# Kernel optimization log

Measured on AMD Instinct MI355X. Metric: run time of the kernel, lower is better.

The kernel has to match this reference:

```python
import jax, jax.numpy as jnp
import numpy as np

N, K, H, W = 2048, 8, 128, 128
G = 50              # glimpse size (50x50 from tem_rnn input 50*50)
ENC = 100           # glimpse encoder output (relation_rnn input arithmetic)
HID = 256
D_REL = ENC + (3 + 50) * 2 + HID          # 462
D_TEM = G * G + (3 + 50) * 2 + HID        # 2862


def _lin(k, out_d, in_d, scale=0.02):
    k1, k2 = jax.random.split(k)
    return (jax.random.normal(k1, (out_d, in_d), jnp.float32) * scale,
            jax.random.normal(k2, (out_d,), jnp.float32) * scale)


def _lstm_params(k, in_d, hid):
    k1, k2, k3, k4 = jax.random.split(k, 4)
    s = 0.02
    return (jax.random.normal(k1, (4 * hid, in_d), jnp.float32) * s,
            jax.random.normal(k2, (4 * hid, hid), jnp.float32) * s,
            jax.random.normal(k3, (4 * hid,), jnp.float32) * s,
            jax.random.normal(k4, (4 * hid,), jnp.float32) * s)


def lstm_cell(x, h, c, Wih, Whh, bih, bhh):
    g = x @ Wih.T + h @ Whh.T + (bih + bhh)
    i, f, gg, o = jnp.split(g, 4, axis=-1)
    i, f, o = jax.nn.sigmoid(i), jax.nn.sigmoid(f), jax.nn.sigmoid(o)
    c2 = f * c + i * jnp.tanh(gg)
    return o * jnp.tanh(c2), c2


def _bilinear_one(im, py, px):
    # im [H,W]; py,px [G,G] pixel coords; zeros padding like torch grid_sample
    x0 = jnp.floor(px); y0 = jnp.floor(py)
    wx1 = px - x0; wy1 = py - y0
    x0i = x0.astype(jnp.int32); y0i = y0.astype(jnp.int32)

    def gather(yi, xi):
        valid = (yi >= 0) & (yi < H) & (xi >= 0) & (xi < W)
        v = im[jnp.clip(yi, 0, H - 1), jnp.clip(xi, 0, W - 1)]
        return jnp.where(valid, v, 0.0)

    return ((1 - wy1) * (1 - wx1) * gather(y0i, x0i)
            + (1 - wy1) * wx1 * gather(y0i, x0i + 1)
            + wy1 * (1 - wx1) * gather(y0i + 1, x0i)
            + wy1 * wx1 * gather(y0i + 1, x0i + 1))


def stn_glimpse(z_where, img):
    # z_where [n,3] = (scale, tx, ty); theta = [[s,0,tx],[0,s,ty]] (attentive_stn_encode)
    s, tx, ty = z_where[:, 0], z_where[:, 1], z_where[:, 2]
    lin = jnp.linspace(-1.0, 1.0, G)
    gy, gx = jnp.meshgrid(lin, lin, indexing='ij')           # [G,G]
    px = (s[:, None, None] * gx + tx[:, None, None] + 1.0) * 0.5 * (W - 1)
    py = (s[:, None, None] * gy + ty[:, None, None] + 1.0) * 0.5 * (H - 1)
    out = jax.vmap(_bilinear_one)(img, py, px)               # [n,G,G]
    return out.reshape(out.shape[0], G * G)


def setup_inputs() -> dict:
    key = jax.random.key(0)
    ks = jax.random.split(key, 16)
    inp = {
        'img': jax.random.uniform(ks[0], (N, H, W), jnp.float32),
        'z_what_last': jax.random.normal(ks[1], (N, K, 50), jnp.float32),
        'z_where_last': jax.random.normal(ks[2], (N, K, 3), jnp.float32) * 0.3,
        'z_pres_last': jnp.ones((N, K, 1), jnp.float32),
        'hidden_last': jax.random.normal(ks[3], (N, K, HID), jnp.float32),
    }
    inp['W_loca'], inp['b_loca'] = _lin(ks[4], 3, HID)
    inp['Wg'], inp['bg'] = _lin(ks[5], ENC, G * G)
    (inp['Wih_rel'], inp['Whh_rel'], inp['bih_rel'], inp['bhh_rel']) = _lstm_params(ks[6], D_REL, HID)
    (inp['Wih_tem'], inp['Whh_tem'], inp['bih_tem'], inp['bhh_tem']) = _lstm_params(ks[7], D_TEM, HID)
    inp['Wm_wh'], inp['bm_wh'] = _lin(ks[8], 3, HID + 3)
    inp['Ws_wh'], inp['bs_wh'] = _lin(ks[9], 3, HID + 3)
    inp['Wm_wt'], inp['bm_wt'] = _lin(ks[10], 50, 50 + HID + HID)
    inp['Ws_wt'], inp['bs_wt'] = _lin(ks[11], 50, 50 + HID + HID)
    inp['Wm_pr'], inp['bm_pr'] = _lin(ks[12], 1, 50 + 3 + HID + HID)
    inp['Ws_pr'], inp['bs_pr'] = _lin(ks[13], 1, 50 + 3 + HID + HID)
    return inp


def reference(img, z_what_last, z_where_last, z_pres_last, hidden_last,
              W_loca, b_loca, Wg, bg,
              Wih_rel, Whh_rel, bih_rel, bhh_rel,
              Wih_tem, Whh_tem, bih_tem, bhh_tem,
              Wm_wh, bm_wh, Ws_wh, bs_wh,
              Wm_wt, bm_wt, Ws_wt, bs_wt,
              Wm_pr, bm_pr, Ws_pr, bs_pr):
    n = img.shape[0]

    def step(carry, xs):
        h_r, c_r, pzw, pzwhat = carry
        zwl, zwhatl, zpl, hl = xs   # [n,3],[n,50],[n,1],[n,256]
        # prop_loca: relu(linear(hidden)) + z_where_last
        zwb = jax.nn.relu(hl @ W_loca.T + b_loca) + zwl
        # STN glimpse + encode (bias pass)
        enc = jax.nn.relu(stn_glimpse(zwb, img) @ Wg.T + bg)        # [n,100]
        rin = jnp.concatenate([enc, zwl, pzw, zwhatl, pzwhat, hl], -1)  # [n,462]
        h_r2, c_r2 = lstm_cell(rin, h_r, c_r, Wih_rel, Whh_rel, bih_rel, bhh_rel)
        # z_where: latent predictor mean (eval mode)
        zw = jnp.concatenate([zwl, h_r2], -1) @ Wm_wh.T + bm_wh      # [n,3]
        # second STN glimpse with sampled where
        g2 = stn_glimpse(zw, img)                                    # [n,2500]
        tin = jnp.concatenate([g2, zw, pzw, zwhatl, pzwhat, hl], -1) # [n,2862]
        h_t, c_t = lstm_cell(tin, h_r2, c_r2, Wih_tem, Whh_tem, bih_tem, bhh_tem)
        # z_what mean
        zwhat = jnp.concatenate([zwhatl, h_r2, h_t], -1) @ Wm_wt.T + bm_wt  # [n,50]
        # z_pres: deterministic expectation of Bernoulli(mean*std) * previous pres
        zp_cal = jnp.concatenate([zwhat, zw, h_r2, h_t], -1)
        p = jax.nn.sigmoid(zp_cal @ Wm_pr.T + bm_pr) * jax.nn.sigmoid(zp_cal @ Ws_pr.T + bs_pr)
        zp = p * zpl                                                 # [n,1]
        return (h_r2, c_r2, zw, zwhat), (zwhat, zw, zp, h_t)

    carry0 = (jnp.zeros((n, HID), img.dtype), jnp.zeros((n, HID), img.dtype),
              jnp.zeros((n, 3), img.dtype), jnp.zeros((n, 50), img.dtype))
    xs = (jnp.swapaxes(z_where_last, 0, 1), jnp.swapaxes(z_what_last, 0, 1),
          jnp.swapaxes(z_pres_last, 0, 1), jnp.swapaxes(hidden_last, 0, 1))
    _, (zwhat_s, zw_s, zp_s, ht_s) = jax.lax.scan(step, carry0, xs)
    z_what = jnp.swapaxes(zwhat_s, 0, 1)   # [n,K,50]
    z_where = jnp.swapaxes(zw_s, 0, 1)     # [n,K,3]
    z_pres = jnp.swapaxes(zp_s, 0, 1)      # [n,K,1]
    h_temp = jnp.swapaxes(ht_s, 0, 1)      # [n,K,256]
    return z_what, z_where, z_pres, h_temp
```

## Files before the change

kernel.cpp:

```cpp
#include <hip/hip_runtime.h>
#include <hip/hip_bf16.h>
#include <math.h>

typedef __attribute__((ext_vector_type(8))) short bf16x8;
typedef __attribute__((ext_vector_type(4))) float f32x4;
using bf16 = __hip_bfloat16;

constexpr int NN   = 2048;
constexpr int KO   = 8;
constexpr int IH   = 128, IW = 128;
constexpr int GS   = 50;
constexpr int GG2  = GS*GS;
constexpr int HIDD = 256;
constexpr int RIN_LD = 768;
constexpr int TIN_LD = 3136;
constexpr int G1_LD  = 2560;

__device__ __forceinline__ float sigm(float x) { return 1.f/(1.f+expf(-x)); }

template<int OUT_BF16, int RELU>
__global__ __launch_bounds__(256, 2) void mfma_gemm(
    const bf16* __restrict__ A, int lda, int Kd,
    const bf16* __restrict__ Wt, int ldw, int M,
    const float* __restrict__ b1, const float* __restrict__ b2,
    void* __restrict__ Cout, int ldc)
{
    __shared__ bf16x8 As16[512];
    __shared__ bf16x8 Bs16[512];
    const int tid  = threadIdx.x;
    const int n0   = blockIdx.y*64;
    const int m0   = blockIdx.x*64;
    const int wave = tid>>6, lane = tid&63;
    const int wy   = wave>>1, wx = wave&1;

    const int row = tid>>2, part = tid&3;
    const bf16* Ap = A + (size_t)(n0+row)*lda + part*8;
    const int   wm = m0 + row;
    const bool  wok = wm < M;
    const bf16* Wp = Wt + (size_t)(wok ? wm : 0)*ldw + part*8;
    const int dst0 = ((row>>4)*2+0)*64 + part*16 + (row&15);
    const int dst1 = dst0 + 64;

    f32x4 acc[2][2] = {};
    const bf16x8 z8 = {};
    bf16x8 pa0 = *(const bf16x8*)Ap;
    bf16x8 pa1 = *(const bf16x8*)(Ap + 32);
    bf16x8 pw0 = *(const bf16x8*)Wp;
    bf16x8 pw1 = *(const bf16x8*)(Wp + 32);

    for (int k0 = 0; k0 < Kd; k0 += 64) {
        __syncthreads();
        As16[dst0] = pa0;
        As16[dst1] = pa1;
        Bs16[dst0] = wok ? pw0 : z8;
        Bs16[dst1] = wok ? pw1 : z8;
        __syncthreads();
        if (k0 + 64 < Kd) {
            pa0 = *(const bf16x8*)(Ap + k0 + 64);
            pa1 = *(const bf16x8*)(Ap + k0 + 96);
            pw0 = *(const bf16x8*)(Wp + k0 + 64);
            pw1 = *(const bf16x8*)(Wp + k0 + 96);
        }
        bf16x8 av[2][2], bv[2][2];
        #pragma unroll
        for (int i=0;i<2;i++)
            #pragma unroll
            for (int h=0;h<2;h++) av[i][h] = As16[((wy*2+i)*2+h)*64 + lane];
        #pragma unroll
        for (int j=0;j<2;j++)
            #pragma unroll
            for (int h=0;h<2;h++) bv[j][h] = Bs16[((wx*2+j)*2+h)*64 + lane];
        #pragma unroll
        for (int h=0;h<2;h++)
            #pragma unroll
            for (int i=0;i<2;i++)
                #pragma unroll
                for (int j=0;j<2;j++)
                    acc[i][j] = __builtin_amdgcn_mfma_f32_16x16x32_bf16(av[i][h], bv[j][h], acc[i][j], 0, 0, 0);
    }

    const int q = lane>>4, r = lane&15;
    #pragma unroll
    for (int j=0;j<2;j++) {
        int col = m0 + wx*32 + j*16 + r;
        if (col < M) {
            float bias = 0.f;
            if (b1) bias += b1[col];
            if (b2) bias += b2[col];
            #pragma unroll
            for (int i=0;i<2;i++) {
                #pragma unroll
                for (int reg=0;reg<4;reg++) {
                    float v = acc[i][j][reg] + bias;
                    if (RELU) v = fmaxf(v, 0.f);
                    size_t idx = (size_t)(n0 + wy*32 + i*16 + q*4 + reg)*ldc + col;
                    if (OUT_BF16) ((bf16*)Cout)[idx] = __float2bfloat16(v);
                    else          ((float*)Cout)[idx] = v;
                }
            }
        }
    }
}

__device__ __forceinline__ void glimpse_points(const float* __restrict__ im,
                                               float s, float tx, float ty,
                                               bf16* __restrict__ drow) {
    const float GXS = 2.0f/49.0f;
    const float txp = tx + 1.0f, typ = ty + 1.0f;
    for (int p2 = threadIdx.x; p2 < 1250; p2 += 256) {
        int i = p2 / 25;
        int j = (p2 - i*25) * 2;
        float gy  = fmaf((float)i, GXS, -1.0f);
        float py  = fmaf(s, gy, typ) * 63.5f;
        float y0f = floorf(py); float fy = py - y0f; int y0 = (int)y0f;
        float wy0 = ((unsigned)y0     < 128u) ? (1.f - fy) : 0.f;
        float wy1 = ((unsigned)(y0+1) < 128u) ? fy         : 0.f;
        const float* r0 = im + min(max(y0,  0),127)*IW;
        const float* r1 = im + min(max(y0+1,0),127)*IW;
        float gxa = fmaf((float)j, GXS, -1.0f);
        float pxa = fmaf(s, gxa, txp) * 63.5f;
        float xa0f = floorf(pxa); float fa = pxa - xa0f; int xa0 = (int)xa0f;
        float wa0 = ((unsigned)xa0     < 128u) ? (1.f - fa) : 0.f;
        float wa1 = ((unsigned)(xa0+1) < 128u) ? fa         : 0.f;
        int xa0c = min(max(xa0,  0),127), xa1c = min(max(xa0+1,0),127);
        float gxb = fmaf((float)(j+1), GXS, -1.0f);
        float pxb = fmaf(s, gxb, txp) * 63.5f;
        float xb0f = floorf(pxb); float fb = pxb - xb0f; int xb0 = (int)xb0f;
        float wb0 = ((unsigned)xb0     < 128u) ? (1.f - fb) : 0.f;
        float wb1 = ((unsigned)(xb0+1) < 128u) ? fb         : 0.f;
        int xb0c = min(max(xb0,  0),127), xb1c = min(max(xb0+1,0),127);

        float va = fmaf(wy1, fmaf(wa0, r1[xa0c], wa1*r1[xa1c]),
                   wy0 *     fmaf(wa0, r0[xa0c], wa1*r0[xa1c]));
        float vb = fmaf(wy1, fmaf(wb0, r1[xb0c], wb1*r1[xb1c]),
                   wy0 *     fmaf(wb0, r0[xb0c], wb1*r0[xb1c]));

        bf16 b0 = __float2bfloat16(va), b1 = __float2bfloat16(vb);
        unsigned short u0, u1;
        __builtin_memcpy(&u0, &b0, 2); __builtin_memcpy(&u1, &b1, 2);
        *(unsigned int*)(drow + i*GS + j) = (unsigned)u0 | ((unsigned)u1 << 16);
    }
}

__global__ __launch_bounds__(256) void glimpse_batch(const float* __restrict__ img,
                                                     const float* __restrict__ z,
                                                     bf16* __restrict__ dst, int ldd) {
    int b = blockIdx.x;
    const float* im = img + (size_t)(b & (NN-1))*IH*IW;
    glimpse_points(im, z[b*3+0], z[b*3+1], z[b*3+2], dst + (size_t)b*ldd);
}

__global__ __launch_bounds__(256) void glimpse2_fused(const float* __restrict__ img,
                                                      const float* __restrict__ zw_cur,
                                                      const float* __restrict__ zw_prev,
                                                      const float* __restrict__ zwhat_prev,
                                                      const float* __restrict__ z_what_last,
                                                      const float* __restrict__ hidden_last,
                                                      bf16* __restrict__ tin, int k) {
    int n = blockIdx.x;
    const float* im = img + (size_t)n*IH*IW;
    float s  = zw_cur[n*3+0];
    float tx = zw_cur[n*3+1];
    float ty = zw_cur[n*3+2];
    bf16* trow = tin + (size_t)n*TIN_LD;
    glimpse_points(im, s, tx, ty, trow);
    for (int c = threadIdx.x; c < 362; c += 256) {
        float v;
        if      (c <   3) v = (c==0) ? s : ((c==1) ? tx : ty);
        else if (c <   6) v = zw_prev[n*3 + c-3];
        else if (c <  56) v = z_what_last[((size_t)n*KO + k)*50 + c-6];
        else if (c < 106) v = zwhat_prev[n*50 + c-56];
        else              v = hidden_last[((size_t)n*KO + k)*HIDD + c-106];
        trow[2500 + c] = __float2bfloat16(v);
    }
}

__global__ void zero_f32(float* __restrict__ p, int n) {
    int i = blockIdx.x*blockDim.x + threadIdx.x;
    if (i < n) p[i] = 0.f;
}

__global__ void repack_w(const float* __restrict__ s1, int K1,
                         const float* __restrict__ s2, int K2,
                         bf16* __restrict__ dst, int ldd, int M) {
    int gid = blockIdx.x*blockDim.x + threadIdx.x;
    if (gid >= M*ldd) return;
    int m = gid / ldd, c = gid - m*ldd;
    float v = 0.f;
    if (c < K1)           v = s1[(size_t)m*K1 + c];
    else if (c < K1+K2)   v = s2[(size_t)m*K2 + (c-K1)];
    dst[gid] = __float2bfloat16(v);
}

__global__ void zwb_all_kernel(const float* __restrict__ hidden_last,
                               const float* __restrict__ z_where_last,
                               const float* __restrict__ Wl, const float* __restrict__ bl,
                               float* __restrict__ zwb_all) {
    int gid = blockIdx.x*blockDim.x + threadIdx.x;
    if (gid >= KO*NN*3) return;
    int j = gid % 3; int rn = gid/3; int n = rn & (NN-1); int s = rn >> 11;
    const float* hl = hidden_last + ((size_t)n*KO + s)*HIDD;
    const float* w  = Wl + j*HIDD;
    float acc = bl[j];
    for (int i=0;i<HIDD;i++) acc = fmaf(hl[i], w[i], acc);
    zwb_all[gid] = fmaxf(acc, 0.f) + z_where_last[((size_t)n*KO + s)*3 + j];
}

__global__ void fill_rin_static(bf16* __restrict__ rin,
                                const float* __restrict__ z_where_last,
                                const float* __restrict__ z_what_last,
                                const float* __restrict__ hidden_last,
                                int base, int CH) {
    int gid = blockIdx.x*blockDim.x + threadIdx.x;
    if (gid >= CH*NN*309) return;
    int c = gid % 309; int rn = gid/309; int n = rn & (NN-1); int sl = rn >> 11;
    int k = base + sl;
    float v; int col;
    if (c < 3)       { col = 100 + c;      v = z_where_last[((size_t)n*KO + k)*3 + c]; }
    else if (c < 53) { col = 106 + (c-3);  v = z_what_last[((size_t)n*KO + k)*50 + (c-3)]; }
    else             { col = 206 + (c-53); v = hidden_last[((size_t)n*KO + k)*HIDD + (c-53)]; }
    rin[(size_t)rn*RIN_LD + col] = __float2bfloat16(v);
}

__global__ void zero_rin_carry(bf16* __restrict__ rin0) {
    int gid = blockIdx.x*blockDim.x + threadIdx.x;
    if (gid >= NN*309) return;
    int c = gid % 309, n = gid/309;
    int col = (c < 3) ? 103+c : ((c < 53) ? 156+(c-3) : 462+(c-53));
    rin0[(size_t)n*RIN_LD + col] = __float2bfloat16(0.f);
}

__global__ __launch_bounds__(256) void rel_fused(
    const float* __restrict__ gates, float* __restrict__ h_r, float* __restrict__ c_r,
    const float* __restrict__ z_where_last,
    const float* __restrict__ Wm_wh, const float* __restrict__ bm_wh,
    float* __restrict__ zw_cur, float* __restrict__ out_zwhere,
    bf16* __restrict__ rin_next, bf16* __restrict__ tin, int k)
{
    __shared__ float hs[256];
    int n = blockIdx.x, j = threadIdx.x;
    const float* g = gates + (size_t)n*1024;
    float ig = sigm(g[j]);
    float fg = sigm(g[256+j]);
    float gg = tanhf(g[512+j]);
    float og = sigm(g[768+j]);
    int cidx = n*256 + j;
    float c2 = fg*c_r[cidx] + ig*gg;
    float hv = og*tanhf(c2);
    c_r[cidx] = c2;
    h_r[cidx] = hv;
    hs[j] = hv;
    bf16 hb = __float2bfloat16(hv);
    rin_next[(size_t)n*RIN_LD + 462 + j] = hb;
    tin[(size_t)n*TIN_LD + 2862 + j]     = hb;
    __syncthreads();
    int w = j >> 6, lane = j & 63;
    if (w < 3) {
        const float* wt = Wm_wh + w*259;
        float s = 0.f;
        for (int i = lane; i < 256; i += 64) s = fmaf(hs[i], wt[3+i], s);
        #pragma unroll
        for (int off = 32; off; off >>= 1) s += __shfl_down(s, off);
        if (lane == 0) {
            const float* zwl = z_where_last + ((size_t)n*KO + k)*3;
            float acc = bm_wh[w] + s;
            for (int i = 0; i < 3; i++) acc = fmaf(zwl[i], wt[i], acc);
            zw_cur[n*3+w] = acc;
            out_zwhere[((size_t)n*KO + k)*3 + w] = acc;
            rin_next[(size_t)n*RIN_LD + 103 + w] = __float2bfloat16(acc);
        }
    }
}

__global__ __launch_bounds__(256) void tem_fused(
    const float* __restrict__ gates, const float* __restrict__ c_r, const float* __restrict__ h_r,
    const float* __restrict__ z_what_last,
    const float* __restrict__ Wm_wt, const float* __restrict__ bm_wt,
    const float* __restrict__ Wm_pr, const float* __restrict__ bm_pr,
    const float* __restrict__ Ws_pr, const float* __restrict__ bs_pr,
    const float* __restrict__ zw_cur, const float* __restrict__ z_pres_last,
    float* __restrict__ zwhat_cur, float* __restrict__ out_zwhat,
    float* __restrict__ out_htemp, float* __restrict__ out_zpres,
    bf16* __restrict__ rin_next, int k)
{
    __shared__ float L[615];
    int n = blockIdx.x, j = threadIdx.x;
    const float* g = gates + (size_t)n*1024;
    float ig = sigm(g[j]);
    float fg = sigm(g[256+j]);
    float gg = tanhf(g[512+j]);
    float og = sigm(g[768+j]);
    float c2 = fg*c_r[n*256+j] + ig*gg;
    float hv = og*tanhf(c2);
    out_htemp[((size_t)n*KO + k)*HIDD + j] = hv;
    L[309+j] = hv;
    L[53+j]  = h_r[n*256+j];
    if (j < 50)      L[j]  = z_what_last[((size_t)n*KO + k)*50 + j];
    else if (j < 53) L[j]  = zw_cur[n*3 + (j-50)];
    __syncthreads();
    if (j < 200) {
        int m = j >> 2, part = j & 3;
        const float* wt = Wm_wt + m*562;
        float s = 0.f;
        for (int i = part; i < 562; i += 4) {
            float v = (i < 50) ? L[i] : L[i+3];
            s = fmaf(v, wt[i], s);
        }
        s += __shfl_down(s, 2);
        s += __shfl_down(s, 1);
        if (part == 0) {
            float acc = s + bm_wt[m];
            zwhat_cur[n*50+m] = acc;
            out_zwhat[((size_t)n*KO + k)*50 + m] = acc;
            rin_next[(size_t)n*RIN_LD + 156 + m] = __float2bfloat16(acc);
            L[565+m] = acc;
        }
    }
    __syncthreads();
    if (j < 64) {
        float s1 = 0.f, s2 = 0.f;
        for (int i = j; i < 565; i += 64) {
            float v = (i < 50) ? L[565+i] : L[i];
            s1 = fmaf(v, Wm_pr[i], s1);
            s2 = fmaf(v, Ws_pr[i], s2);
        }
        #pragma unroll
        for (int off = 32; off; off >>= 1) { s1 += __shfl_down(s1,off); s2 += __shfl_down(s2,off); }
        if (j == 0) {
            float p = sigm(s1 + bm_pr[0]) * sigm(s2 + bs_pr[0]);
            out_zpres[(size_t)n*KO + k] = p * z_pres_last[(size_t)n*KO + k];
        }
    }
}

extern "C" void kernel_launch(void* const* d_in, const int* in_sizes, int n_in,
                              void* d_out, int out_size, void* d_ws, size_t ws_size,
                              hipStream_t stream) {
    (void)in_sizes; (void)n_in; (void)out_size;
    const float* img          = (const float*)d_in[0];
    const float* z_what_last  = (const float*)d_in[1];
    const float* z_where_last = (const float*)d_in[2];
    const float* z_pres_last  = (const float*)d_in[3];
    const float* hidden_last  = (const float*)d_in[4];
    const float* W_loca = (const float*)d_in[5];
    const float* b_loca = (const float*)d_in[6];
    const float* Wg     = (const float*)d_in[7];
    const float* bg     = (const float*)d_in[8];
    const float* Wih_rel = (const float*)d_in[9];
    const float* Whh_rel = (const float*)d_in[10];
    const float* bih_rel = (const float*)d_in[11];
    const float* bhh_rel = (const float*)d_in[12];
    const float* Wih_tem = (const float*)d_in[13];
    const float* Whh_tem = (const float*)d_in[14];
    const float* bih_tem = (const float*)d_in[15];
    const float* bhh_tem = (const float*)d_in[16];
    const float* Wm_wh = (const float*)d_in[17];
    const float* bm_wh = (const float*)d_in[18];
    const float* Wm_wt = (const float*)d_in[21];
    const float* bm_wt = (const float*)d_in[22];
    const float* Wm_pr = (const float*)d_in[25];
    const float* bm_pr = (const float*)d_in[26];
    const float* Ws_pr = (const float*)d_in[27];
    const float* bs_pr = (const float*)d_in[28];

    char* base_p = (char*)d_ws;
    size_t off = 0;
    auto carve = [&](size_t bytes) -> char* {
        char* r = base_p + off;
        off += (bytes + 255) & ~(size_t)255;
        return r;
    };
    bf16*  tin      = (bf16*) carve((size_t)NN*TIN_LD*2);
    float* gates    = (float*)carve((size_t)NN*1024*4);
    bf16*  W_tem    = (bf16*) carve((size_t)1024*TIN_LD*2);
    bf16*  W_rel    = (bf16*) carve((size_t)1024*RIN_LD*2);
    bf16*  Wg_bf    = (bf16*) carve((size_t)100*G1_LD*2);
    float* zwb_all  = (float*)carve((size_t)KO*NN*3*4);
    float* h_r      = (float*)carve((size_t)NN*HIDD*4);
    float* c_r      = (float*)carve((size_t)NN*HIDD*4);
    float* zw1      = (float*)carve((size_t)NN*3*4);
    float* zwhat1   = (float*)carve((size_t)NN*50*4);
    float* zw0      = (float*)carve((size_t)NN*3*4);
    float* zwhat0   = (float*)carve((size_t)NN*50*4);
    size_t fixed_bytes = off;

    int CH = 1;
    for (int cand : {8, 4, 2}) {
        size_t need = fixed_bytes
                    + (((size_t)cand*NN*G1_LD*2 + 255) & ~(size_t)255)
                    + (((size_t)cand*NN*RIN_LD*2 + 255) & ~(size_t)255);
        if (need <= ws_size) { CH = cand; break; }
    }
    bf16* g1 = nullptr; int g1ld;
    bf16* rin;
    if (CH > 1) {
        g1   = (bf16*)carve((size_t)CH*NN*G1_LD*2);
        rin  = (bf16*)carve((size_t)CH*NN*RIN_LD*2);
        g1ld = G1_LD;
    } else {
        rin  = (bf16*)carve((size_t)NN*RIN_LD*2);
        g1   = tin;
        g1ld = TIN_LD;
    }

    float* out        = (float*)d_out;
    float* out_zwhat  = out;
    float* out_zwhere = out + (size_t)NN*KO*50;
    float* out_zpres  = out_zwhere + (size_t)NN*KO*3;
    float* out_htemp  = out_zpres + (size_t)NN*KO;

    {
        int nz = NN*(HIDD + 3 + 50);
        zero_f32<<<(nz+255)/256, 256, 0, stream>>>(c_r, nz);
    }
    zero_rin_carry<<<(NN*309+255)/256, 256, 0, stream>>>(rin);
    repack_w<<<((1024*RIN_LD)+255)/256, 256, 0, stream>>>(Wih_rel, 462, Whh_rel, 256, W_rel, RIN_LD, 1024);
    repack_w<<<((1024*TIN_LD)+255)/256, 256, 0, stream>>>(Wih_tem, 2862, Whh_tem, 256, W_tem, TIN_LD, 1024);
    repack_w<<<((100*G1_LD)+255)/256, 256, 0, stream>>>(Wg, 2500, nullptr, 0, Wg_bf, G1_LD, 100);
    zwb_all_kernel<<<(KO*NN*3+255)/256, 256, 0, stream>>>(hidden_last, z_where_last, W_loca, b_loca, zwb_all);

    for (int cbase = 0; cbase < KO; cbase += CH) {
        fill_rin_static<<<(CH*NN*309+255)/256, 256, 0, stream>>>(rin, z_where_last, z_what_last, hidden_last, cbase, CH);
        glimpse_batch<<<CH*NN, 256, 0, stream>>>(img, zwb_all + (size_t)cbase*NN*3, g1, g1ld);
        mfma_gemm<1,1><<<dim3(2, CH*32), 256, 0, stream>>>(g1, g1ld, G1_LD, Wg_bf, G1_LD, 100, bg, nullptr, rin, RIN_LD);

        for (int s = 0; s < CH; ++s) {
            int k = cbase + s;
            bf16* rin_k  = rin + (size_t)s*NN*RIN_LD;
            bf16* rin_nx = rin + (size_t)((s+1)%CH)*NN*RIN_LD;
            float* zw_cur     = (k & 1) ? zw1 : zw0;
            float* zw_prev    = (k & 1) ? zw0 : zw1;
            float* zwhat_cur  = (k & 1) ? zwhat1 : zwhat0;
            float* zwhat_prev = (k & 1) ? zwhat0 : zwhat1;

            mfma_gemm<0,0><<<dim3(16, 32), 256, 0, stream>>>(rin_k, RIN_LD, RIN_LD, W_rel, RIN_LD, 1024, bih_rel, bhh_rel, gates, 1024);
            rel_fused<<<NN, 256, 0, stream>>>(gates, h_r, c_r, z_where_last, Wm_wh, bm_wh, zw_cur, out_zwhere, rin_nx, tin, k);
            glimpse2_fused<<<NN, 256, 0, stream>>>(img, zw_cur, zw_prev, zwhat_prev, z_what_last, hidden_last, tin, k);
            mfma_gemm<0,0><<<dim3(16, 32), 256, 0, stream>>>(tin, TIN_LD, TIN_LD, W_tem, TIN_LD, 1024, bih_tem, bhh_tem, gates, 1024);
            tem_fused<<<NN, 256, 0, stream>>>(gates, c_r, h_r, z_what_last, Wm_wt, bm_wt, Wm_pr, bm_pr, Ws_pr, bs_pr,
                                              zw_cur, z_pres_last, zwhat_cur, out_zwhat, out_htemp, out_zpres, rin_nx, k);
        }
    }
}
```

Measured before the change: 1.348 ms.

## Fuse LSTM gate epilogue into GEMM and stage glimpse rows in LDS

The LSTM weight rows are reordered so each 64-column GEMM tile holds all four gates for 16 hidden units. The gate nonlinearities and cell update then run in the GEMM epilogue, which removes the fp32 gates buffer round trip and the separate rel/tem elementwise kernels. The z_where projection moves into the glimpse kernel. Glimpse sampling first copies the needed image rows into shared memory, and zwb_all is rewritten as a wave reduction. The cost is more shared memory per block, which may lower occupancy, and an extra epilogue sync in the GEMM.

```diff
diff --git a/kernel.cpp b/kernel.cpp
--- a/kernel.cpp
+++ b/kernel.cpp
@@ -10,23 +10,30 @@
 constexpr int KO   = 8;
 constexpr int IH   = 128, IW = 128;
 constexpr int GS   = 50;
-constexpr int GG2  = GS*GS;
 constexpr int HIDD = 256;
 constexpr int RIN_LD = 768;
 constexpr int TIN_LD = 3136;
 constexpr int G1_LD  = 2560;
+constexpr int GROWS  = 80;
 
 __device__ __forceinline__ float sigm(float x) { return 1.f/(1.f+expf(-x)); }
 
-template<int OUT_BF16, int RELU>
+template<int MODE>
 __global__ __launch_bounds__(256, 2) void mfma_gemm(
     const bf16* __restrict__ A, int lda, int Kd,
     const bf16* __restrict__ Wt, int ldw, int M,
     const float* __restrict__ b1, const float* __restrict__ b2,
-    void* __restrict__ Cout, int ldc)
+    const float* __restrict__ bint,
+    void* __restrict__ Cout, int ldc,
+    float* __restrict__ c_r, float* __restrict__ h_out,
+    bf16* __restrict__ rin_next, bf16* __restrict__ tin_,
+    float* __restrict__ out_htemp, int kstep)
 {
-    __shared__ bf16x8 As16[512];
-    __shared__ bf16x8 Bs16[512];
+    __shared__ __align__(16) char shraw[68*64*4];
+    bf16x8* As16 = (bf16x8*)shraw;
+    bf16x8* Bs16 = As16 + 512;
+    float*  Gt   = (float*)shraw;
+
     const int tid  = threadIdx.x;
     const int n0   = blockIdx.y*64;
     const int m0   = blockIdx.x*64;
@@ -80,94 +87,197 @@
     }
 
     const int q = lane>>4, r = lane&15;
-    #pragma unroll
-    for (int j=0;j<2;j++) {
-        int col = m0 + wx*32 + j*16 + r;
-        if (col < M) {
-            float bias = 0.f;
-            if (b1) bias += b1[col];
-            if (b2) bias += b2[col];
+    if (MODE == 1) {
+        #pragma unroll
+        for (int j=0;j<2;j++) {
+            int col = m0 + wx*32 + j*16 + r;
+            if (col < M) {
+                float bias = 0.f;
+                if (b1) bias += b1[col];
+                if (b2) bias += b2[col];
+                #pragma unroll
+                for (int i=0;i<2;i++)
+                    #pragma unroll
+                    for (int reg=0;reg<4;reg++) {
+                        float v = fmaxf(acc[i][j][reg] + bias, 0.f);
+                        ((bf16*)Cout)[(size_t)(n0 + wy*32 + i*16 + q*4 + reg)*ldc + col] = __float2bfloat16(v);
+                    }
+            }
+        }
+    } else {
+        __syncthreads();
+        #pragma unroll
+        for (int j=0;j<2;j++) {
+            int colL = wx*32 + j*16 + r;
+            float bias = bint[m0 + colL];
             #pragma unroll
-            for (int i=0;i<2;i++) {
+            for (int i=0;i<2;i++)
                 #pragma unroll
-                for (int reg=0;reg<4;reg++) {
-                    float v = acc[i][j][reg] + bias;
-                    if (RELU) v = fmaxf(v, 0.f);
-                    size_t idx = (size_t)(n0 + wy*32 + i*16 + q*4 + reg)*ldc + col;
-                    if (OUT_BF16) ((bf16*)Cout)[idx] = __float2bfloat16(v);
-                    else          ((float*)Cout)[idx] = v;
-                }
+                for (int reg=0;reg<4;reg++)
+                    Gt[(wy*32 + i*16 + q*4 + reg)*68 + colL] = acc[i][j][reg] + bias;
+        }
+        __syncthreads();
+        #pragma unroll
+        for (int it=0; it<4; ++it) {
+            int item = tid + it*256;
+            int rowL = item >> 4, u16 = item & 15;
+            f32x4 gv = *(const f32x4*)&Gt[rowL*68 + u16*4];
+            float ig = sigm(gv[0]);
+            float fg = sigm(gv[1]);
+            float gg = tanhf(gv[2]);
+            float og = sigm(gv[3]);
+            int n = n0 + rowL, u = (m0>>2) + u16;
+            size_t cidx = (size_t)n*HIDD + u;
+            float c2 = fg*c_r[cidx] + ig*gg;
+            float hv = og*tanhf(c2);
+            if (MODE == 2) {
+                c_r[cidx] = c2;
+                h_out[cidx] = hv;
+                bf16 hb = __float2bfloat16(hv);
+                rin_next[(size_t)n*RIN_LD + 462 + u] = hb;
+                tin_[(size_t)n*TIN_LD + 2862 + u]    = hb;
+            } else {
+                h_out[cidx] = hv;
+                out_htemp[((size_t)n*KO + kstep)*HIDD + u] = hv;
             }
         }
     }
 }
 
-__device__ __forceinline__ void glimpse_points(const float* __restrict__ im,
-                                               float s, float tx, float ty,
-                                               bf16* __restrict__ drow) {
+__device__ __forceinline__ void glimpse_core(const float* __restrict__ im,
+                                             float s, float tx, float ty,
+                                             bf16* __restrict__ drow,
+                                             float* __restrict__ rows) {
     const float GXS = 2.0f/49.0f;
     const float txp = tx + 1.0f, typ = ty + 1.0f;
-    for (int p2 = threadIdx.x; p2 < 1250; p2 += 256) {
-        int i = p2 / 25;
-        int j = (p2 - i*25) * 2;
-        float gy  = fmaf((float)i, GXS, -1.0f);
-        float py  = fmaf(s, gy, typ) * 63.5f;
-        float y0f = floorf(py); float fy = py - y0f; int y0 = (int)y0f;
-        float wy0 = ((unsigned)y0     < 128u) ? (1.f - fy) : 0.f;
-        float wy1 = ((unsigned)(y0+1) < 128u) ? fy         : 0.f;
-        const float* r0 = im + min(max(y0,  0),127)*IW;
-        const float* r1 = im + min(max(y0+1,0),127)*IW;
-        float gxa = fmaf((float)j, GXS, -1.0f);
-        float pxa = fmaf(s, gxa, txp) * 63.5f;
-        float xa0f = floorf(pxa); float fa = pxa - xa0f; int xa0 = (int)xa0f;
-        float wa0 = ((unsigned)xa0     < 128u) ? (1.f - fa) : 0.f;
-        float wa1 = ((unsigned)(xa0+1) < 128u) ? fa         : 0.f;
-        int xa0c = min(max(xa0,  0),127), xa1c = min(max(xa0+1,0),127);
-        float gxb = fmaf((float)(j+1), GXS, -1.0f);
-        float pxb = fmaf(s, gxb, txp) * 63.5f;
-        float xb0f = floorf(pxb); float fb = pxb - xb0f; int xb0 = (int)xb0f;
-        float wb0 = ((unsigned)xb0     < 128u) ? (1.f - fb) : 0.f;
-        float wb1 = ((unsigned)(xb0+1) < 128u) ? fb         : 0.f;
-        int xb0c = min(max(xb0,  0),127), xb1c = min(max(xb0+1,0),127);
-
-        float va = fmaf(wy1, fmaf(wa0, r1[xa0c], wa1*r1[xa1c]),
-                   wy0 *     fmaf(wa0, r0[xa0c], wa1*r0[xa1c]));
-        float vb = fmaf(wy1, fmaf(wb0, r1[xb0c], wb1*r1[xb1c]),
-                   wy0 *     fmaf(wb0, r0[xb0c], wb1*r0[xb1c]));
-
-        bf16 b0 = __float2bfloat16(va), b1 = __float2bfloat16(vb);
-        unsigned short u0, u1;
-        __builtin_memcpy(&u0, &b0, 2); __builtin_memcpy(&u1, &b1, 2);
-        *(unsigned int*)(drow + i*GS + j) = (unsigned)u0 | ((unsigned)u1 << 16);
+    float pyA = fmaf(s, -1.f, typ)*63.5f;
+    float pyB = fmaf(s,  1.f, typ)*63.5f;
+    int ylo = (int)floorf(fminf(pyA, pyB));
+    int yhi = (int)floorf(fmaxf(pyA, pyB)) + 1;
+    ylo = min(max(ylo, 0), 127);
+    yhi = min(max(yhi, 0), 127);
+    int nrows = yhi - ylo + 1;
+
+    if (nrows <= GROWS) {
+        const float4* src = (const float4*)(im + ylo*IW);
+        float4* d4 = (float4*)rows;
+        int tot = nrows*(IW/4);
+        for (int t = threadIdx.x; t < tot; t += 256) d4[t] = src[t];
+        __syncthreads();
+        for (int p2 = threadIdx.x; p2 < 1250; p2 += 256) {
+            int i = p2 / 25, j = (p2 - i*25)*2;
+            float gy  = fmaf((float)i, GXS, -1.0f);
+            float py  = fmaf(s, gy, typ)*63.5f;
+            float y0f = floorf(py); float fy = py - y0f; int y0 = (int)y0f;
+            float wy0 = ((unsigned)y0     < 128u) ? (1.f - fy) : 0.f;
+            float wy1 = ((unsigned)(y0+1) < 128u) ? fy         : 0.f;
+            const float* r0 = rows + min(max(y0-ylo,   0), nrows-1)*IW;
+            const float* r1 = rows + min(max(y0+1-ylo, 0), nrows-1)*IW;
+            float gxa = fmaf((float)j, GXS, -1.0f);
+            float pxa = fmaf(s, gxa, txp)*63.5f;
+            float xa0f = floorf(pxa); float fa = pxa - xa0f; int xa0 = (int)xa0f;
+            float wa0 = ((unsigned)xa0     < 128u) ? (1.f - fa) : 0.f;
+            float wa1 = ((unsigned)(xa0+1) < 128u) ? fa         : 0.f;
+            int xa0c = min(max(xa0,  0),127), xa1c = min(max(xa0+1,0),127);
+            float gxb = fmaf((float)(j+1), GXS, -1.0f);
+            float pxb = fmaf(s, gxb, txp)*63.5f;
+            float xb0f = floorf(pxb); float fb = pxb - xb0f; int xb0 = (int)xb0f;
+            float wb0 = ((unsigned)xb0     < 128u) ? (1.f - fb) : 0.f;
+            float wb1 = ((unsigned)(xb0+1) < 128u) ? fb         : 0.f;
+            int xb0c = min(max(xb0,  0),127), xb1c = min(max(xb0+1,0),127);
+            float va = fmaf(wy1, fmaf(wa0, r1[xa0c], wa1*r1[xa1c]),
+                       wy0 *     fmaf(wa0, r0[xa0c], wa1*r0[xa1c]));
+            float vb = fmaf(wy1, fmaf(wb0, r1[xb0c], wb1*r1[xb1c]),
+                       wy0 *     fmaf(wb0, r0[xb0c], wb1*r0[xb1c]));
+            bf16 b0 = __float2bfloat16(va), b1 = __float2bfloat16(vb);
+            unsigned short u0, u1;
+            __builtin_memcpy(&u0, &b0, 2); __builtin_memcpy(&u1, &b1, 2);
+            *(unsigned int*)(drow + i*GS + j) = (unsigned)u0 | ((unsigned)u1 << 16);
+        }
+    } else {
+        for (int p2 = threadIdx.x; p2 < 1250; p2 += 256) {
+            int i = p2 / 25, j = (p2 - i*25)*2;
+            float gy  = fmaf((float)i, GXS, -1.0f);
+            float py  = fmaf(s, gy, typ)*63.5f;
+            float y0f = floorf(py); float fy = py - y0f; int y0 = (int)y0f;
+            float wy0 = ((unsigned)y0     < 128u) ? (1.f - fy) : 0.f;
+            float wy1 = ((unsigned)(y0+1) < 128u) ? fy         : 0.f;
+            const float* r0 = im + min(max(y0,  0),127)*IW;
+            const float* r1 = im + min(max(y0+1,0),127)*IW;
+            float gxa = fmaf((float)j, GXS, -1.0f);
+            float pxa = fmaf(s, gxa, txp)*63.5f;
+            float xa0f = floorf(pxa); float fa = pxa - xa0f; int xa0 = (int)xa0f;
+            float wa0 = ((unsigned)xa0     < 128u) ? (1.f - fa) : 0.f;
+            float wa1 = ((unsigned)(xa0+1) < 128u) ? fa         : 0.f;
+            int xa0c = min(max(xa0,  0),127), xa1c = min(max(xa0+1,0),127);
+            float gxb = fmaf((float)(j+1), GXS, -1.0f);
+            float pxb = fmaf(s, gxb, txp)*63.5f;
+            float xb0f = floorf(pxb); float fb = pxb - xb0f; int xb0 = (int)xb0f;
+            float wb0 = ((unsigned)xb0     < 128u) ? (1.f - fb) : 0.f;
+            float wb1 = ((unsigned)(xb0+1) < 128u) ? fb         : 0.f;
+            int xb0c = min(max(xb0,  0),127), xb1c = min(max(xb0+1,0),127);
+            float va = fmaf(wy1, fmaf(wa0, r1[xa0c], wa1*r1[xa1c]),
+                       wy0 *     fmaf(wa0, r0[xa0c], wa1*r0[xa1c]));
+            float vb = fmaf(wy1, fmaf(wb0, r1[xb0c], wb1*r1[xb1c]),
+                       wy0 *     fmaf(wb0, r0[xb0c], wb1*r0[xb1c]));
+            bf16 b0 = __float2bfloat16(va), b1 = __float2bfloat16(vb);
+            unsigned short u0, u1;
+            __builtin_memcpy(&u0, &b0, 2); __builtin_memcpy(&u1, &b1, 2);
+            *(unsigned int*)(drow + i*GS + j) = (unsigned)u0 | ((unsigned)u1 << 16);
+        }
     }
 }
 
 __global__ __launch_bounds__(256) void glimpse_batch(const float* __restrict__ img,
                                                      const float* __restrict__ z,
                                                      bf16* __restrict__ dst, int ldd) {
+    __shared__ float rows[GROWS*IW];
     int b = blockIdx.x;
     const float* im = img + (size_t)(b & (NN-1))*IH*IW;
-    glimpse_points(im, z[b*3+0], z[b*3+1], z[b*3+2], dst + (size_t)b*ldd);
-}
-
-__global__ __launch_bounds__(256) void glimpse2_fused(const float* __restrict__ img,
-                                                      const float* __restrict__ zw_cur,
-                                                      const float* __restrict__ zw_prev,
-                                                      const float* __restrict__ zwhat_prev,
-                                                      const float* __restrict__ z_what_last,
-                                                      const float* __restrict__ hidden_last,
-                                                      bf16* __restrict__ tin, int k) {
-    int n = blockIdx.x;
-    const float* im = img + (size_t)n*IH*IW;
-    float s  = zw_cur[n*3+0];
-    float tx = zw_cur[n*3+1];
-    float ty = zw_cur[n*3+2];
+    glimpse_core(im, z[b*3+0], z[b*3+1], z[b*3+2], dst + (size_t)b*ldd, rows);
+}
+
+__global__ __launch_bounds__(256) void glimpse2_zw(
+    const float* __restrict__ img, const float* __restrict__ h_r,
+    const float* __restrict__ z_where_last,
+    const float* __restrict__ Wm_wh, const float* __restrict__ bm_wh,
+    const float* __restrict__ zw_prev, const float* __restrict__ zwhat_prev,
+    const float* __restrict__ z_what_last, const float* __restrict__ hidden_last,
+    float* __restrict__ zw_cur, float* __restrict__ out_zwhere,
+    bf16* __restrict__ tin, bf16* __restrict__ rin_next, int k)
+{
+    __shared__ float rows[GROWS*IW];
+    __shared__ float hsv[HIDD];
+    __shared__ float zws[3];
+    int n = blockIdx.x, tid = threadIdx.x;
+    hsv[tid] = h_r[(size_t)n*HIDD + tid];
+    __syncthreads();
+    int wv = tid>>6, lane = tid&63;
+    if (wv < 3) {
+        const float* wt = Wm_wh + wv*259;
+        float sa = 0.f;
+        for (int i = lane; i < 256; i += 64) sa = fmaf(hsv[i], wt[3+i], sa);
+        #pragma unroll
+        for (int off=32; off; off>>=1) sa += __shfl_down(sa, off);
+        if (lane == 0) {
+            const float* zwl = z_where_last + ((size_t)n*KO + k)*3;
+            float acc = bm_wh[wv] + sa;
+            for (int i=0;i<3;i++) acc = fmaf(zwl[i], wt[i], acc);
+            zws[wv] = acc;
+            zw_cur[n*3+wv] = acc;
+            out_zwhere[((size_t)n*KO + k)*3 + wv] = acc;
+            bf16 ab = __float2bfloat16(acc);
+            rin_next[(size_t)n*RIN_LD + 103 + wv] = ab;
+            tin[(size_t)n*TIN_LD + 2500 + wv]     = ab;
+        }
+    }
+    __syncthreads();
+    float s = zws[0], tx = zws[1], ty = zws[2];
     bf16* trow = tin + (size_t)n*TIN_LD;
-    glimpse_points(im, s, tx, ty, trow);
-    for (int c = threadIdx.x; c < 362; c += 256) {
+    glimpse_core(img + (size_t)n*IH*IW, s, tx, ty, trow, rows);
+    for (int c = 3 + tid; c < 362; c += 256) {
         float v;
-        if      (c <   3) v = (c==0) ? s : ((c==1) ? tx : ty);
-        else if (c <   6) v = zw_prev[n*3 + c-3];
+        if      (c <   6) v = zw_prev[n*3 + c-3];
         else if (c <  56) v = z_what_last[((size_t)n*KO + k)*50 + c-6];
         else if (c < 106) v = zwhat_prev[n*50 + c-56];
         else              v = hidden_last[((size_t)n*KO + k)*HIDD + c-106];
@@ -192,18 +302,59 @@
     dst[gid] = __float2bfloat16(v);
 }
 
-__global__ void zwb_all_kernel(const float* __restrict__ hidden_last,
-                               const float* __restrict__ z_where_last,
-                               const float* __restrict__ Wl, const float* __restrict__ bl,
-                               float* __restrict__ zwb_all) {
+__global__ void repack_w_gates(const float* __restrict__ s1, int K1,
+                               const float* __restrict__ s2, int K2,
+                               bf16* __restrict__ dst, int ldd) {
     int gid = blockIdx.x*blockDim.x + threadIdx.x;
-    if (gid >= KO*NN*3) return;
-    int j = gid % 3; int rn = gid/3; int n = rn & (NN-1); int s = rn >> 11;
+    if (gid >= 1024*ldd) return;
+    int mp = gid / ldd, c = gid - mp*ldd;
+    int u = mp >> 2, g = mp & 3;
+    int m = g*256 + u;
+    float v = 0.f;
+    if (c < K1)           v = s1[(size_t)m*K1 + c];
+    else if (c < K1+K2)   v = s2[(size_t)m*K2 + (c-K1)];
+    dst[gid] = __float2bfloat16(v);
+}
+
+__global__ void repack_bias_gates(const float* __restrict__ b1, const float* __restrict__ b2,
+                                  float* __restrict__ dst) {
+    int mp = blockIdx.x*blockDim.x + threadIdx.x;
+    if (mp >= 1024) return;
+    int u = mp >> 2, g = mp & 3;
+    dst[mp] = b1[g*256+u] + b2[g*256+u];
+}
+
+__global__ __launch_bounds__(256) void zwb_all_v2(const float* __restrict__ hidden_last,
+                                                  const float* __restrict__ z_where_last,
+                                                  const float* __restrict__ Wl, const float* __restrict__ bl,
+                                                  float* __restrict__ zwb_all) {
+    __shared__ float wls[768];
+    for (int i = threadIdx.x; i < 768; i += 256) wls[i] = Wl[i];
+    __syncthreads();
+    int wv = threadIdx.x>>6, lane = threadIdx.x&63;
+    int row = blockIdx.x*4 + wv;
+    int s = row >> 11, n = row & (NN-1);
     const float* hl = hidden_last + ((size_t)n*KO + s)*HIDD;
-    const float* w  = Wl + j*HIDD;
-    float acc = bl[j];
-    for (int i=0;i<HIDD;i++) acc = fmaf(hl[i], w[i], acc);
-    zwb_all[gid] = fmaxf(acc, 0.f) + z_where_last[((size_t)n*KO + s)*3 + j];
+    float4 h4 = *(const float4*)(hl + lane*4);
+    float s0=0.f, s1=0.f, s2=0.f;
+    #pragma unroll
+    for (int r4=0;r4<4;r4++) {
+        float hv = ((const float*)&h4)[r4];
+        int i = lane*4 + r4;
+        s0 = fmaf(hv, wls[i],     s0);
+        s1 = fmaf(hv, wls[256+i], s1);
+        s2 = fmaf(hv, wls[512+i], s2);
+    }
+    #pragma unroll
+    for (int off=32; off; off>>=1) {
+        s0 += __shfl_down(s0,off); s1 += __shfl_down(s1,off); s2 += __shfl_down(s2,off);
+    }
+    if (lane == 0) {
+        const float* zwl = z_where_last + ((size_t)n*KO + s)*3;
+        zwb_all[row*3+0] = fmaxf(s0+bl[0],0.f) + zwl[0];
+        zwb_all[row*3+1] = fmaxf(s1+bl[1],0.f) + zwl[1];
+        zwb_all[row*3+2] = fmaxf(s2+bl[2],0.f) + zwl[2];
+    }
 }
 
 __global__ void fill_rin_static(bf16* __restrict__ rin,
@@ -230,86 +381,35 @@
     rin0[(size_t)n*RIN_LD + col] = __float2bfloat16(0.f);
 }
 
-__global__ __launch_bounds__(256) void rel_fused(
-    const float* __restrict__ gates, float* __restrict__ h_r, float* __restrict__ c_r,
-    const float* __restrict__ z_where_last,
-    const float* __restrict__ Wm_wh, const float* __restrict__ bm_wh,
-    float* __restrict__ zw_cur, float* __restrict__ out_zwhere,
-    bf16* __restrict__ rin_next, bf16* __restrict__ tin, int k)
-{
-    __shared__ float hs[256];
-    int n = blockIdx.x, j = threadIdx.x;
-    const float* g = gates + (size_t)n*1024;
-    float ig = sigm(g[j]);
-    float fg = sigm(g[256+j]);
-    float gg = tanhf(g[512+j]);
-    float og = sigm(g[768+j]);
-    int cidx = n*256 + j;
-    float c2 = fg*c_r[cidx] + ig*gg;
-    float hv = og*tanhf(c2);
-    c_r[cidx] = c2;
-    h_r[cidx] = hv;
-    hs[j] = hv;
-    bf16 hb = __float2bfloat16(hv);
-    rin_next[(size_t)n*RIN_LD + 462 + j] = hb;
-    tin[(size_t)n*TIN_LD + 2862 + j]     = hb;
-    __syncthreads();
-    int w = j >> 6, lane = j & 63;
-    if (w < 3) {
-        const float* wt = Wm_wh + w*259;
-        float s = 0.f;
-        for (int i = lane; i < 256; i += 64) s = fmaf(hs[i], wt[3+i], s);
-        #pragma unroll
-        for (int off = 32; off; off >>= 1) s += __shfl_down(s, off);
-        if (lane == 0) {
-            const float* zwl = z_where_last + ((size_t)n*KO + k)*3;
-            float acc = bm_wh[w] + s;
-            for (int i = 0; i < 3; i++) acc = fmaf(zwl[i], wt[i], acc);
-            zw_cur[n*3+w] = acc;
-            out_zwhere[((size_t)n*KO + k)*3 + w] = acc;
-            rin_next[(size_t)n*RIN_LD + 103 + w] = __float2bfloat16(acc);
-        }
-    }
-}
-
-__global__ __launch_bounds__(256) void tem_fused(
-    const float* __restrict__ gates, const float* __restrict__ c_r, const float* __restrict__ h_r,
+__global__ __launch_bounds__(256) void tem_tail(
+    const float* __restrict__ h_r, const float* __restrict__ h_t,
     const float* __restrict__ z_what_last,
     const float* __restrict__ Wm_wt, const float* __restrict__ bm_wt,
     const float* __restrict__ Wm_pr, const float* __restrict__ bm_pr,
     const float* __restrict__ Ws_pr, const float* __restrict__ bs_pr,
     const float* __restrict__ zw_cur, const float* __restrict__ z_pres_last,
     float* __restrict__ zwhat_cur, float* __restrict__ out_zwhat,
-    float* __restrict__ out_htemp, float* __restrict__ out_zpres,
-    bf16* __restrict__ rin_next, int k)
+    float* __restrict__ out_zpres, bf16* __restrict__ rin_next, int k)
 {
     __shared__ float L[615];
     int n = blockIdx.x, j = threadIdx.x;
-    const float* g = gates + (size_t)n*1024;
-    float ig = sigm(g[j]);
-    float fg = sigm(g[256+j]);
-    float gg = tanhf(g[512+j]);
-    float og = sigm(g[768+j]);
-    float c2 = fg*c_r[n*256+j] + ig*gg;
-    float hv = og*tanhf(c2);
-    out_htemp[((size_t)n*KO + k)*HIDD + j] = hv;
-    L[309+j] = hv;
-    L[53+j]  = h_r[n*256+j];
-    if (j < 50)      L[j]  = z_what_last[((size_t)n*KO + k)*50 + j];
-    else if (j < 53) L[j]  = zw_cur[n*3 + (j-50)];
+    L[309+j] = h_t[(size_t)n*HIDD + j];
+    L[53+j]  = h_r[(size_t)n*HIDD + j];
+    if (j < 50)      L[j] = z_what_last[((size_t)n*KO + k)*50 + j];
+    else if (j < 53) L[j] = zw_cur[n*3 + (j-50)];
     __syncthreads();
     if (j < 200) {
         int m = j >> 2, part = j & 3;
         const float* wt = Wm_wt + m*562;
-        float s = 0.f;
+        float sa = 0.f;
         for (int i = part; i < 562; i += 4) {
             float v = (i < 50) ? L[i] : L[i+3];
-            s = fmaf(v, wt[i], s);
-        }
-        s += __shfl_down(s, 2);
-        s += __shfl_down(s, 1);
+            sa = fmaf(v, wt[i], sa);
+        }
+        sa += __shfl_down(sa, 2);
+        sa += __shfl_down(sa, 1);
         if (part == 0) {
-            float acc = s + bm_wt[m];
+            float acc = sa + bm_wt[m];
             zwhat_cur[n*50+m] = acc;
             out_zwhat[((size_t)n*KO + k)*50 + m] = acc;
             rin_next[(size_t)n*RIN_LD + 156 + m] = __float2bfloat16(acc);
@@ -371,12 +471,14 @@
         return r;
     };
     bf16*  tin      = (bf16*) carve((size_t)NN*TIN_LD*2);
-    float* gates    = (float*)carve((size_t)NN*1024*4);
     bf16*  W_tem    = (bf16*) carve((size_t)1024*TIN_LD*2);
     bf16*  W_rel    = (bf16*) carve((size_t)1024*RIN_LD*2);
     bf16*  Wg_bf    = (bf16*) carve((size_t)100*G1_LD*2);
+    float* bint_rel = (float*)carve(1024*4);
+    float* bint_tem = (float*)carve(1024*4);
     float* zwb_all  = (float*)carve((size_t)KO*NN*3*4);
     float* h_r      = (float*)carve((size_t)NN*HIDD*4);
+    float* h_t      = (float*)carve((size_t)NN*HIDD*4);
     float* c_r      = (float*)carve((size_t)NN*HIDD*4);
     float* zw1      = (float*)carve((size_t)NN*3*4);
     float* zwhat1   = (float*)carve((size_t)NN*50*4);
@@ -414,15 +516,18 @@
         zero_f32<<<(nz+255)/256, 256, 0, stream>>>(c_r, nz);
     }
     zero_rin_carry<<<(NN*309+255)/256, 256, 0, stream>>>(rin);
-    repack_w<<<((1024*RIN_LD)+255)/256, 256, 0, stream>>>(Wih_rel, 462, Whh_rel, 256, W_rel, RIN_LD, 1024);
-    repack_w<<<((1024*TIN_LD)+255)/256, 256, 0, stream>>>(Wih_tem, 2862, Whh_tem, 256, W_tem, TIN_LD, 1024);
+    repack_w_gates<<<((1024*RIN_LD)+255)/256, 256, 0, stream>>>(Wih_rel, 462, Whh_rel, 256, W_rel, RIN_LD);
+    repack_w_gates<<<((1024*TIN_LD)+255)/256, 256, 0, stream>>>(Wih_tem, 2862, Whh_tem, 256, W_tem, TIN_LD);
     repack_w<<<((100*G1_LD)+255)/256, 256, 0, stream>>>(Wg, 2500, nullptr, 0, Wg_bf, G1_LD, 100);
-    zwb_all_kernel<<<(KO*NN*3+255)/256, 256, 0, stream>>>(hidden_last, z_where_last, W_loca, b_loca, zwb_all);
+    repack_bias_gates<<<4, 256, 0, stream>>>(bih_rel, bhh_rel, bint_rel);
+    repack_bias_gates<<<4, 256, 0, stream>>>(bih_tem, bhh_tem, bint_tem);
+    zwb_all_v2<<<KO*NN/4, 256, 0, stream>>>(hidden_last, z_where_last, W_loca, b_loca, zwb_all);
 
     for (int cbase = 0; cbase < KO; cbase += CH) {
         fill_rin_static<<<(CH*NN*309+255)/256, 256, 0, stream>>>(rin, z_where_last, z_what_last, hidden_last, cbase, CH);
         glimpse_batch<<<CH*NN, 256, 0, stream>>>(img, zwb_all + (size_t)cbase*NN*3, g1, g1ld);
-        mfma_gemm<1,1><<<dim3(2, CH*32), 256, 0, stream>>>(g1, g1ld, G1_LD, Wg_bf, G1_LD, 100, bg, nullptr, rin, RIN_LD);
+        mfma_gemm<1><<<dim3(2, CH*32), 256, 0, stream>>>(g1, g1ld, G1_LD, Wg_bf, G1_LD, 100,
+            bg, nullptr, nullptr, rin, RIN_LD, nullptr, nullptr, nullptr, nullptr, nullptr, 0);
 
         for (int s = 0; s < CH; ++s) {
             int k = cbase + s;
@@ -433,12 +538,15 @@
             float* zwhat_cur  = (k & 1) ? zwhat1 : zwhat0;
             float* zwhat_prev = (k & 1) ? zwhat0 : zwhat1;
 
-            mfma_gemm<0,0><<<dim3(16, 32), 256, 0, stream>>>(rin_k, RIN_LD, RIN_LD, W_rel, RIN_LD, 1024, bih_rel, bhh_rel, gates, 1024);
-            rel_fused<<<NN, 256, 0, stream>>>(gates, h_r, c_r, z_where_last, Wm_wh, bm_wh, zw_cur, out_zwhere, rin_nx, tin, k);
-            glimpse2_fused<<<NN, 256, 0, stream>>>(img, zw_cur, zw_prev, zwhat_prev, z_what_last, hidden_last, tin, k);
-            mfma_gemm<0,0><<<dim3(16, 32), 256, 0, stream>>>(tin, TIN_LD, TIN_LD, W_tem, TIN_LD, 1024, bih_tem, bhh_tem, gates, 1024);
-            tem_fused<<<NN, 256, 0, stream>>>(gates, c_r, h_r, z_what_last, Wm_wt, bm_wt, Wm_pr, bm_pr, Ws_pr, bs_pr,
-                                              zw_cur, z_pres_last, zwhat_cur, out_zwhat, out_htemp, out_zpres, rin_nx, k);
-        }
-    }
-}
+            mfma_gemm<2><<<dim3(16, 32), 256, 0, stream>>>(rin_k, RIN_LD, RIN_LD, W_rel, RIN_LD, 1024,
+                nullptr, nullptr, bint_rel, nullptr, 0, c_r, h_r, rin_nx, tin, nullptr, k);
+            glimpse2_zw<<<NN, 256, 0, stream>>>(img, h_r, z_where_last, Wm_wh, bm_wh,
+                zw_prev, zwhat_prev, z_what_last, hidden_last, zw_cur, out_zwhere, tin, rin_nx, k);
+            mfma_gemm<3><<<dim3(16, 32), 256, 0, stream>>>(tin, TIN_LD, TIN_LD, W_tem, TIN_LD, 1024,
+                nullptr, nullptr, bint_tem, nullptr, 0, c_r, h_t, nullptr, nullptr, out_htemp, k);
+            tem_tail<<<NN, 256, 0, stream>>>(h_r, h_t, z_what_last, Wm_wt, bm_wt,
+                Wm_pr, bm_pr, Ws_pr, bs_pr, zw_cur, z_pres_last,
+                zwhat_cur, out_zwhat, out_zpres, rin_nx, k);
+        }
+    }
+}
```

Result: slower. 1.377 ms (+2.2%).
